# Optimization experiments

Measured on AMD Instinct MI355X. Metric: run time of the kernel, lower is better.

The kernel has to match this reference:

```python
import jax, jax.numpy as jnp
import numpy as np

B, C, H, W = 16, 256, 32, 32
NUM_LAYERS = 30
OUT = 16  # sqrt(out_channels)
EPS = 1e-5


def setup_inputs() -> dict:
    key = jax.random.key(0)
    k1, k2, k3 = jax.random.split(key, 3)
    x = jax.random.normal(k1, (B, C, H, W), dtype=jnp.float32)
    # delta_t ~ small positive values (module inits ~N(0.01, 0.005))
    delta_t = jax.random.uniform(k2, (NUM_LAYERS, 1), dtype=jnp.float32) * 0.02
    matrices = jax.random.normal(k3, (NUM_LAYERS, 1, 1, OUT, OUT), dtype=jnp.float32) * 0.1
    gamma = jnp.ones((H * W,), dtype=jnp.float32)   # BatchNorm2d weight, oc = i*i = H*W
    beta = jnp.zeros((H * W,), dtype=jnp.float32)   # BatchNorm2d bias
    return {"x": x, "delta_t": delta_t, "matrices": matrices, "gamma": gamma, "beta": beta}


def _bn_relu6(z, gamma, beta):
    # training-mode BatchNorm2d over channel axis 1 (channels = H*W), then ReLU6
    mean = jnp.mean(z, axis=(0, 2, 3), keepdims=True)
    var = jnp.mean(jnp.square(z - mean), axis=(0, 2, 3), keepdims=True)  # biased var
    zhat = (z - mean) * jax.lax.rsqrt(var + EPS)
    g = gamma.reshape(1, -1, 1, 1)
    b = beta.reshape(1, -1, 1, 1)
    return jnp.clip(zhat * g + b, 0.0, 6.0)


def reference(x, delta_t, matrices, gamma, beta):
    b, c, h, w = x.shape
    hw = h * w
    # feature_reshape: [B,C,H,W] -> [B,HW,C] -> [B,HW,out,out] (inn == out branch)
    x1 = x.reshape(b, c, hw).transpose(0, 2, 1).reshape(b, hw, OUT, OUT)
    dt = jnp.clip(delta_t, 0.0, 6.0)[:, 0]  # relu6(delta_t), shape [L]

    def step(y0, params):
        m, dtl = params  # m: [1,1,out,out] broadcasts elementwise against x1
        dydt = -y0 + _bn_relu6(y0 + m * x1, gamma, beta)
        return y0 + dtl * dydt, None

    y0, _ = jax.lax.scan(step, x1, (matrices, dt))
    # (y0 + x1): [B, HW, out, out] -> view [B,H,W,out*out] -> permute to [B,out*out,H,W]
    y = (y0 + x1).reshape(b, h, w, OUT * OUT).transpose(0, 3, 1, 2)
    return y
```

## Files before the change

### kernel.cpp

```cpp
#include <hip/hip_runtime.h>

#define HW      1024
#define BC      4096
#define NLAYERS 30

__global__ __launch_bounds__(256) void transpose_k(const float* __restrict__ src,
                                                   float* __restrict__ dst,
                                                   int R, int C) {
    __shared__ float tile[32][33];
    const int cb = blockIdx.x * 32;
    const int rb = blockIdx.y * 32;
    const int tx = threadIdx.x;
    const int ty = threadIdx.y;
#pragma unroll
    for (int k = 0; k < 32; k += 8)
        tile[ty + k][tx] = src[(size_t)(rb + ty + k) * C + (cb + tx)];
    __syncthreads();
#pragma unroll
    for (int k = 0; k < 32; k += 8)
        dst[(size_t)(cb + ty + k) * R + (rb + tx)] = tile[tx][ty + k];
}

__global__ __launch_bounds__(256) void ode_main(const float* __restrict__ xT,
                                                const float* __restrict__ delta_t,
                                                const float* __restrict__ matrices,
                                                const float* __restrict__ gamma,
                                                const float* __restrict__ beta,
                                                float* __restrict__ yT) {
    const int p = blockIdx.x;
    const int t = threadIdx.x;
    const float* xrow = xT + (size_t)p * BC;

    float x1[16], y[16];
#pragma unroll
    for (int j = 0; j < 4; ++j) {
        const float4 v = *(const float4*)(xrow + j * 1024 + 4 * t);
        x1[j * 4 + 0] = v.x; x1[j * 4 + 1] = v.y;
        x1[j * 4 + 2] = v.z; x1[j * 4 + 3] = v.w;
    }
#pragma unroll
    for (int k = 0; k < 16; ++k) y[k] = x1[k];

    const float gp = gamma[p];
    const float bp = beta[p];
    const int   wid  = t >> 6;
    const int   lane = t & 63;
    const int   moff = (4 * t) & 255;

    __shared__ float red[2][8];

    for (int l = 0; l < NLAYERS; ++l) {
        const float4 mv = *(const float4*)(matrices + l * 256 + moff);
        const float mm[4] = {mv.x, mv.y, mv.z, mv.w};
        const float dtl = fminf(fmaxf(delta_t[l], 0.0f), 6.0f);

        float z[16];
        float s = 0.0f, s2 = 0.0f;
#pragma unroll
        for (int j = 0; j < 4; ++j) {
#pragma unroll
            for (int i = 0; i < 4; ++i) {
                const float zz = fmaf(mm[i], x1[j * 4 + i], y[j * 4 + i]);
                z[j * 4 + i] = zz;
                s  += zz;
                s2  = fmaf(zz, zz, s2);
            }
        }
#pragma unroll
        for (int mask = 1; mask < 64; mask <<= 1) {
            s  += __shfl_xor(s,  mask, 64);
            s2 += __shfl_xor(s2, mask, 64);
        }
        const int par = l & 1;
        if (lane == 0) { red[par][wid * 2] = s; red[par][wid * 2 + 1] = s2; }
        __syncthreads();
        const float S  = red[par][0] + red[par][2] + red[par][4] + red[par][6];
        const float S2 = red[par][1] + red[par][3] + red[par][5] + red[par][7];

        const float mean = S * (1.0f / 4096.0f);
        const float var  = fmaf(-mean, mean, S2 * (1.0f / 4096.0f));
        const float rstd = rsqrtf(var + 1e-5f);
        const float g    = gp * rstd;
        const float bb   = fmaf(-mean, g, bp);
        const float omdt = 1.0f - dtl;
#pragma unroll
        for (int k = 0; k < 16; ++k) {
            float a = fmaf(z[k], g, bb);
            a = fminf(fmaxf(a, 0.0f), 6.0f);
            y[k] = fmaf(dtl, a, omdt * y[k]);
        }
    }

    float* yrow = yT + (size_t)p * BC;
#pragma unroll
    for (int j = 0; j < 4; ++j) {
        float4 w;
        w.x = y[j * 4 + 0] + x1[j * 4 + 0];
        w.y = y[j * 4 + 1] + x1[j * 4 + 1];
        w.z = y[j * 4 + 2] + x1[j * 4 + 2];
        w.w = y[j * 4 + 3] + x1[j * 4 + 3];
        *(float4*)(yrow + j * 1024 + 4 * t) = w;
    }
}

extern "C" void kernel_launch(void* const* d_in, const int* in_sizes, int n_in,
                              void* d_out, int out_size, void* d_ws, size_t ws_size,
                              hipStream_t stream) {
    const float* x        = (const float*)d_in[0];
    const float* delta_t  = (const float*)d_in[1];
    const float* matrices = (const float*)d_in[2];
    const float* gamma    = (const float*)d_in[3];
    const float* beta     = (const float*)d_in[4];
    float* out = (float*)d_out;

    float* xT = out;
    float* yT = (float*)d_ws;

    dim3 blk(32, 8);
    transpose_k<<<dim3(HW / 32, BC / 32), blk, 0, stream>>>(x, xT, BC, HW);
    ode_main<<<dim3(HW), dim3(256), 0, stream>>>(xT, delta_t, matrices, gamma, beta, yT);
    transpose_k<<<dim3(BC / 32, HW / 32), blk, 0, stream>>>(yT, out, HW, BC);
}
```

Baseline: 126.2 us.

## Fuse input and output transposes into the ODE kernel with strided global access

Drops the two separate tiled-transpose kernels and the workspace round-trip. The ODE kernel now reads x and writes out directly in NCHW layout, with each thread handling the channels t+256k for one spatial position. The per-layer matrices and delta_t are preloaded into shared memory, and the clamp uses med3. This saves two launches and about 64MB of extra global traffic. In exchange, the global loads and stores are strided by HW floats across threads, so they are uncoalesced and depend on L2 to merge neighbouring blocks' accesses.

```diff
diff --git a/kernel.cpp b/kernel.cpp
--- a/kernel.cpp
+++ b/kernel.cpp
@@ -3,68 +3,53 @@
 #define HW      1024
 #define BC      4096
 #define NLAYERS 30
+#define TPB     256
 
-__global__ __launch_bounds__(256) void transpose_k(const float* __restrict__ src,
-                                                   float* __restrict__ dst,
-                                                   int R, int C) {
-    __shared__ float tile[32][33];
-    const int cb = blockIdx.x * 32;
-    const int rb = blockIdx.y * 32;
-    const int tx = threadIdx.x;
-    const int ty = threadIdx.y;
-#pragma unroll
-    for (int k = 0; k < 32; k += 8)
-        tile[ty + k][tx] = src[(size_t)(rb + ty + k) * C + (cb + tx)];
-    __syncthreads();
-#pragma unroll
-    for (int k = 0; k < 32; k += 8)
-        dst[(size_t)(cb + ty + k) * R + (rb + tx)] = tile[tx][ty + k];
-}
-
-__global__ __launch_bounds__(256) void ode_main(const float* __restrict__ xT,
-                                                const float* __restrict__ delta_t,
-                                                const float* __restrict__ matrices,
-                                                const float* __restrict__ gamma,
-                                                const float* __restrict__ beta,
-                                                float* __restrict__ yT) {
+__global__ __launch_bounds__(TPB) void ode_fused(const float* __restrict__ x,
+                                                 const float* __restrict__ delta_t,
+                                                 const float* __restrict__ matrices,
+                                                 const float* __restrict__ gamma,
+                                                 const float* __restrict__ beta,
+                                                 float* __restrict__ out) {
     const int p = blockIdx.x;
     const int t = threadIdx.x;
-    const float* xrow = xT + (size_t)p * BC;
+
+    __shared__ float smat[NLAYERS * 256];
+    __shared__ float sdt[NLAYERS];
+    __shared__ float red[2][8];
+
+#pragma unroll
+    for (int i = 0; i < NLAYERS; ++i)
+        smat[i * 256 + t] = matrices[i * 256 + t];
+    if (t < NLAYERS)
+        sdt[t] = __builtin_amdgcn_fmed3f(delta_t[t], 0.0f, 6.0f);
 
     float x1[16], y[16];
 #pragma unroll
-    for (int j = 0; j < 4; ++j) {
-        const float4 v = *(const float4*)(xrow + j * 1024 + 4 * t);
-        x1[j * 4 + 0] = v.x; x1[j * 4 + 1] = v.y;
-        x1[j * 4 + 2] = v.z; x1[j * 4 + 3] = v.w;
-    }
+    for (int k = 0; k < 16; ++k)
+        x1[k] = x[(size_t)(t + 256 * k) * HW + p];
 #pragma unroll
     for (int k = 0; k < 16; ++k) y[k] = x1[k];
 
-    const float gp = gamma[p];
-    const float bp = beta[p];
+    const float gp   = gamma[p];
+    const float bp   = beta[p];
     const int   wid  = t >> 6;
     const int   lane = t & 63;
-    const int   moff = (4 * t) & 255;
 
-    __shared__ float red[2][8];
+    __syncthreads();
 
     for (int l = 0; l < NLAYERS; ++l) {
-        const float4 mv = *(const float4*)(matrices + l * 256 + moff);
-        const float mm[4] = {mv.x, mv.y, mv.z, mv.w};
-        const float dtl = fminf(fmaxf(delta_t[l], 0.0f), 6.0f);
+        const float m   = smat[l * 256 + t];
+        const float dtl = sdt[l];
 
         float z[16];
         float s = 0.0f, s2 = 0.0f;
 #pragma unroll
-        for (int j = 0; j < 4; ++j) {
-#pragma unroll
-            for (int i = 0; i < 4; ++i) {
-                const float zz = fmaf(mm[i], x1[j * 4 + i], y[j * 4 + i]);
-                z[j * 4 + i] = zz;
-                s  += zz;
-                s2  = fmaf(zz, zz, s2);
-            }
+        for (int k = 0; k < 16; ++k) {
+            const float zz = fmaf(m, x1[k], y[k]);
+            z[k] = zz;
+            s += zz;
+            s2 = fmaf(zz, zz, s2);
         }
 #pragma unroll
         for (int mask = 1; mask < 64; mask <<= 1) {
@@ -85,22 +70,14 @@
         const float omdt = 1.0f - dtl;
 #pragma unroll
         for (int k = 0; k < 16; ++k) {
-            float a = fmaf(z[k], g, bb);
-            a = fminf(fmaxf(a, 0.0f), 6.0f);
+            const float a = __builtin_amdgcn_fmed3f(fmaf(z[k], g, bb), 0.0f, 6.0f);
             y[k] = fmaf(dtl, a, omdt * y[k]);
         }
     }
 
-    float* yrow = yT + (size_t)p * BC;
 #pragma unroll
-    for (int j = 0; j < 4; ++j) {
-        float4 w;
-        w.x = y[j * 4 + 0] + x1[j * 4 + 0];
-        w.y = y[j * 4 + 1] + x1[j * 4 + 1];
-        w.z = y[j * 4 + 2] + x1[j * 4 + 2];
-        w.w = y[j * 4 + 3] + x1[j * 4 + 3];
-        *(float4*)(yrow + j * 1024 + 4 * t) = w;
-    }
+    for (int k = 0; k < 16; ++k)
+        out[(size_t)(t + 256 * k) * HW + p] = y[k] + x1[k];
 }
 
 extern "C" void kernel_launch(void* const* d_in, const int* in_sizes, int n_in,
@@ -113,11 +90,5 @@
     const float* beta     = (const float*)d_in[4];
     float* out = (float*)d_out;
 
-    float* xT = out;
-    float* yT = (float*)d_ws;
-
-    dim3 blk(32, 8);
-    transpose_k<<<dim3(HW / 32, BC / 32), blk, 0, stream>>>(x, xT, BC, HW);
-    ode_main<<<dim3(HW), dim3(256), 0, stream>>>(xT, delta_t, matrices, gamma, beta, yT);
-    transpose_k<<<dim3(BC / 32, HW / 32), blk, 0, stream>>>(yT, out, HW, BC);
+    ode_fused<<<dim3(HW), dim3(TPB), 0, stream>>>(x, delta_t, matrices, gamma, beta, out);
 }
```

After: 133.5 us. 1.06x slower.
